# Performance work log

Hardware: AMD Instinct MI355X
Metric: run time of the kernel (lower is better)

Reference implementation:

```python
import jax, jax.numpy as jnp
import numpy as np

MASK_RADIUS = 30.0

def _fft_mask(height, width, mode):
    # replicates fft_filter_def: grid over full H rows and rfft half-plane cols
    cht, cwt = height // 2, width // 2
    fy, fx = jnp.meshgrid(jnp.arange(height), jnp.arange(width // 2 + 1), indexing='ij')
    dist = jnp.sqrt((fx - cwt).astype(jnp.float32) ** 2 + (fy - cht).astype(jnp.float32) ** 2)
    if mode == 'high':
        return (dist > MASK_RADIUS).astype(jnp.float32)
    return (dist <= MASK_RADIUS).astype(jnp.float32)


def setup_inputs() -> dict:
    key = jax.random.key(0)
    k1, k2, k3 = jax.random.split(key, 3)
    B, Cin, Cout, H, W, K = 4, 64, 64, 128, 128, 3
    x = jax.random.normal(k1, (B, Cin, H, W), dtype=jnp.float32)
    weight = jax.random.normal(k2, (Cout, Cin, K, K), dtype=jnp.float32) * 0.1
    bias = jax.random.normal(k3, (Cout,), dtype=jnp.float32) * 0.1
    return {"x": x, "weight": weight, "bias": bias}


def reference(x, weight, bias):
    B, Cin, H, W = x.shape
    x = x.astype(jnp.float32)
    # rfft2 of input, then fftshift (as in original; kernel FFT is NOT shifted)
    fft_x = jnp.fft.rfft2(x)                          # [B, Cin, H, W//2+1]
    fft_x = jnp.fft.fftshift(fft_x, axes=(-2, -1))
    kernel_fft = jnp.fft.rfft2(weight, s=(H, W))      # [Cout, Cin, H, W//2+1]
    # high-pass frequency mask (fft_filter == 'high')
    mask = _fft_mask(H, W, 'high')                    # [H, W//2+1]
    fft_x = fft_x * mask
    # per-frequency complex GEMV over in_channels (avoids [B,Cout,Cin,H,Wf] blowup)
    fft_out = jnp.einsum('bihw,oihw->bohw', fft_x, kernel_fft)
    out = jnp.fft.irfft2(fft_out, s=(H, W))           # [B, Cout, H, W]
    return out + bias[None, :, None, None]
```

## Files before the change

### kernel.cpp

```cpp
#include <hip/hip_runtime.h>

#define PI_F 3.14159265358979323846f

#define HH 128
#define WW 128
#define WF 65
#define NB 4
#define NC 64
#define CPLX_PER_IMG (HH * WF)

typedef __attribute__((ext_vector_type(8))) short short8;
typedef __attribute__((ext_vector_type(4))) float f32x4;

__device__ __forceinline__ ushort f2b(float f) {
    unsigned u = __float_as_uint(f);
    u += 0x7fffu + ((u >> 16) & 1u);
    return (ushort)(u >> 16);
}


__global__ __launch_bounds__(256) void k_pre(const float* __restrict__ w,
                                             ushort* __restrict__ A1,
                                             ushort* __restrict__ A2,
                                             ushort* __restrict__ A4,
                                             ushort* __restrict__ A5,
                                             ushort* __restrict__ WvRe,
                                             ushort* __restrict__ WvIm) {
    int idx = blockIdx.x * 256 + threadIdx.x;
    if (idx < 20480) {
        int m = idx >> 7, k = idx & 127;
        int part = m / 80, v = m - part * 80;
        float s, c;
        __sincosf(2.f * PI_F * (float)((v * k) & 127) / 128.f, &s, &c);
        float val = (v < 65) ? (part ? -s : c) : 0.f;
        A1[idx] = f2b(val);
    } else if (idx < 86016) {
        int j = idx - 20480;
        int m = j >> 8, k2 = j & 255;
        int part = m >> 7, u = m & 127;
        int kp = k2 >> 7, h = k2 & 127;
        float s, c;
        __sincosf(2.f * PI_F * (float)((u * h) & 127) / 128.f, &s, &c);
        float val = part == 0 ? (kp == 0 ? c : s) : (kp == 0 ? -s : c);
        A2[j] = f2b(val);
    } else if (idx < 151552) {
        int j = idx - 86016;
        int m = j >> 8, k2 = j & 255;
        int part = m >> 7, h = m & 127;
        int kp = k2 >> 7, u = k2 & 127;
        float s, c;
        __sincosf(2.f * PI_F * (float)((u * h) & 127) / 128.f, &s, &c);
        float val = part == 0 ? (kp == 0 ? c : -s) : (kp == 0 ? s : c);
        A4[j] = f2b(val * (1.f / 128.f));
    } else if (idx < 172032) {
        int j = idx - 151552;
        int x = j / 160, k2 = j - x * 160;
        int part = k2 / 80, v = k2 - part * 80;
        float s, c;
        __sincosf(2.f * PI_F * (float)((v * x) & 127) / 128.f, &s, &c);
        float cv = (v == 0 || v == 64) ? 1.f : 2.f;
        float val = (v < 65) ? (part == 0 ? cv * c : -cv * s) * (1.f / 128.f) : 0.f;
        A5[j] = f2b(val);
    } else {
        int xw = idx - 172032;
        int i = xw & 63;
        int o = (xw >> 6) & 63;
        int pv = xw >> 12;
        int p = pv / WF;
        int v = pv % WF;
        const float* wp = w + ((size_t)o * 64 + i) * 9 + p * 3;
        float re = wp[0], im = 0.f;
#pragma unroll
        for (int q = 1; q <= 2; ++q) {
            int k = (v * q) & 127;
            float s, c;
            __sincosf(-2.f * PI_F * (float)k / 128.f, &s, &c);
            re += wp[q] * c;
            im += wp[q] * s;
        }
        WvRe[xw] = f2b(re);
        WvIm[xw] = f2b(im);
    }
}

#define B1P 136
#define B2P 280
__global__ __launch_bounds__(1024) void k_fwd(const float* __restrict__ x,
                                              const ushort* __restrict__ A1,
                                              const ushort* __restrict__ A2,
                                              ushort* __restrict__ XsRe,
                                              ushort* __restrict__ XsIm) {
    __shared__ ushort B1[128 * B1P];
    __shared__ ushort B2[80 * B2P];
    int t = threadIdx.x;
    int img = blockIdx.x;
    const float* gx = x + (size_t)img * 16384;
    for (int c = t; c < 2048; c += 1024) {
        int r = c >> 4, sl = c & 15;
        const float* src = gx + r * 128 + sl * 8;
        float4 f0 = *(const float4*)src;
        float4 f1 = *(const float4*)(src + 4);
        short8 v8;
        v8[0] = (short)f2b(f0.x); v8[1] = (short)f2b(f0.y);
        v8[2] = (short)f2b(f0.z); v8[3] = (short)f2b(f0.w);
        v8[4] = (short)f2b(f1.x); v8[5] = (short)f2b(f1.y);
        v8[6] = (short)f2b(f1.z); v8[7] = (short)f2b(f1.w);
        *(short8*)&B1[r * B1P + sl * 8] = v8;
    }
    __syncthreads();
    int lane = t & 63, wave = t >> 6;
    int lrow = lane & 15, lq = lane >> 4;

    {
        int g = wave >> 3, nt = wave & 7;
        int hrow = nt * 16 + lrow;
        f32x4 acc[5];
#pragma unroll
        for (int j = 0; j < 5; ++j) acc[j] = (f32x4){0.f, 0.f, 0.f, 0.f};
#pragma unroll
        for (int ks = 0; ks < 4; ++ks) {
            short8 b = *(short8*)&B1[hrow * B1P + ks * 32 + lq * 8];
#pragma unroll
            for (int j = 0; j < 5; ++j) {
                int mt = g * 5 + j;
                short8 a = *(const short8*)&A1[(mt * 16 + lrow) * 128 + ks * 32 + lq * 8];
                acc[j] = __builtin_amdgcn_mfma_f32_16x16x32_bf16(a, b, acc[j], 0, 0, 0);
            }
        }
#pragma unroll
        for (int j = 0; j < 5; ++j) {
            int m0 = (g * 5 + j) * 16 + lq * 4;
            int part = m0 >= 80;
            int v0 = m0 - part * 80;
#pragma unroll
            for (int e = 0; e < 4; ++e)
                B2[(v0 + e) * B2P + part * 128 + hrow] = f2b(acc[j][e]);
        }
    }
    __syncthreads();

    {
        int nt = wave;
        f32x4 acc[5];
#pragma unroll
        for (int mt = 0; mt < 5; ++mt) acc[mt] = (f32x4){0.f, 0.f, 0.f, 0.f};
#pragma unroll
        for (int ks = 0; ks < 8; ++ks) {
            short8 b = *(const short8*)&A2[(nt * 16 + lrow) * 256 + ks * 32 + lq * 8];
#pragma unroll
            for (int mt = 0; mt < 5; ++mt) {
                short8 a = *(short8*)&B2[(mt * 16 + lrow) * B2P + ks * 32 + lq * 8];
                acc[mt] = __builtin_amdgcn_mfma_f32_16x16x32_bf16(a, b, acc[mt], 0, 0, 0);
            }
        }
        int part = nt >= 8;
        int u = (nt & 7) * 16 + lrow;
        int u_out = (u + 64) & 127;
        int du = u_out - 64;
        ushort* dimg = (part ? XsIm : XsRe) + (size_t)img * CPLX_PER_IMG;
#pragma unroll
        for (int mt = 0; mt < 5; ++mt)
#pragma unroll
            for (int e = 0; e < 4; ++e) {
                int v_in = mt * 16 + lq * 4 + e;
                if (v_in < 65) {
                    int v_out = v_in + 32; if (v_out >= 65) v_out -= 65;
                    int dv = v_out - 64;
                    bool keep = (du * du + dv * dv) > 900;
                    dimg[v_out * 128 + u_out] = keep ? f2b(acc[mt][e]) : (ushort)0;
                }
            }
    }
}

#define AP 72
__global__ __launch_bounds__(256, 2) void k_gemm(const ushort* __restrict__ XsRe,
                                                 const ushort* __restrict__ XsIm,
                                                 const ushort* __restrict__ WvRe,
                                                 const ushort* __restrict__ WvIm,
                                                 ushort* __restrict__ Zre,
                                                 ushort* __restrict__ Zim) {
    __shared__ ushort XTre[128 * AP], XTim[128 * AP];
    __shared__ ushort WSre[64 * AP],  WSim[64 * AP];
    int t = threadIdx.x;
    int v = blockIdx.x >> 2;
    int b = blockIdx.x & 3;
    {
        int u = t & 127, qh = t >> 7;
#pragma unroll
        for (int q8 = 0; q8 < 8; ++q8) {
            int q = qh * 8 + q8;
            ushort re4[4], im4[4];
#pragma unroll
            for (int c = 0; c < 4; ++c) {
                int i = q * 4 + c;
                size_t off = ((size_t)(b * 64 + i) * WF + v) * 128 + u;
                re4[c] = XsRe[off];
                im4[c] = XsIm[off];
            }
            *(ushort4*)&XTre[u * AP + q * 4] = make_ushort4(re4[0], re4[1], re4[2], re4[3]);
            *(ushort4*)&XTim[u * AP + q * 4] = make_ushort4(im4[0], im4[1], im4[2], im4[3]);
        }
    }
    int lane = t & 63, wave = t >> 6;
    int lrow = lane & 15, lq = lane >> 4;
    int u0 = wave * 32;
    f32x4 fRe[8], fIm[8];
#pragma unroll
    for (int m = 0; m < 8; ++m) {
        fRe[m] = (f32x4){0.f, 0.f, 0.f, 0.f};
        fIm[m] = (f32x4){0.f, 0.f, 0.f, 0.f};
    }
    for (int p = 0; p < 3; ++p) {
        if (p) __syncthreads();
        {
            const ushort* gr = WvRe + ((size_t)(p * WF + v)) * 4096;
            const ushort* gi = WvIm + ((size_t)(p * WF + v)) * 4096;
#pragma unroll
            for (int cc = 0; cc < 2; ++cc) {
                int c = t + cc * 256;
                int o = c >> 3, i0 = (c & 7) * 8;
                *(short8*)&WSre[o * AP + i0] = *(const short8*)&gr[c * 8];
                *(short8*)&WSim[o * AP + i0] = *(const short8*)&gi[c * 8];
            }
        }
        __syncthreads();
        f32x4 pRe[8], pIm[8];
#pragma unroll
        for (int m = 0; m < 8; ++m) {
            pRe[m] = (f32x4){0.f, 0.f, 0.f, 0.f};
            pIm[m] = (f32x4){0.f, 0.f, 0.f, 0.f};
        }
#pragma unroll
        for (int ks = 0; ks < 2; ++ks) {
            int kb = ks * 32 + lq * 8;
            short8 br[2], bi[2], bin[2];
#pragma unroll
            for (int ut = 0; ut < 2; ++ut) {
                int u = u0 + ut * 16 + lrow;
                br[ut] = *(const short8*)&XTre[u * AP + kb];
                bi[ut] = *(const short8*)&XTim[u * AP + kb];
                bin[ut] = bi[ut] ^ (short)0x8000;
            }
#pragma unroll
            for (int ot = 0; ot < 4; ++ot) {
                int o = ot * 16 + lrow;
                short8 ar = *(const short8*)&WSre[o * AP + kb];
                short8 ai = *(const short8*)&WSim[o * AP + kb];
#pragma unroll
                for (int ut = 0; ut < 2; ++ut) {
                    int m = ot * 2 + ut;
                    pRe[m] = __builtin_amdgcn_mfma_f32_16x16x32_bf16(ai, bin[ut], pRe[m], 0, 0, 0);
                    pRe[m] = __builtin_amdgcn_mfma_f32_16x16x32_bf16(ar, br[ut],  pRe[m], 0, 0, 0);
                    pIm[m] = __builtin_amdgcn_mfma_f32_16x16x32_bf16(ai, br[ut],  pIm[m], 0, 0, 0);
                    pIm[m] = __builtin_amdgcn_mfma_f32_16x16x32_bf16(ar, bi[ut],  pIm[m], 0, 0, 0);
                }
            }
        }
#pragma unroll
        for (int ut = 0; ut < 2; ++ut) {
            int u = u0 + ut * 16 + lrow;
            float sn, cn;
            __sincosf(-2.f * PI_F * (float)(u * p) / 128.f, &sn, &cn);
#pragma unroll
            for (int ot = 0; ot < 4; ++ot) {
                int m = ot * 2 + ut;
#pragma unroll
                for (int e = 0; e < 4; ++e) {
                    fRe[m][e] += pRe[m][e] * cn - pIm[m][e] * sn;
                    fIm[m][e] += pIm[m][e] * cn + pRe[m][e] * sn;
                }
            }
        }
    }
#pragma unroll
    for (int ot = 0; ot < 4; ++ot)
#pragma unroll
        for (int ut = 0; ut < 2; ++ut) {
            int m = ot * 2 + ut;
            int u = u0 + ut * 16 + lrow;
#pragma unroll
            for (int e = 0; e < 4; ++e) {
                int o = ot * 16 + lq * 4 + e;
                size_t idx = ((size_t)(b * 64 + o) * 65 + v) * 128 + u;
                Zre[idx] = f2b(fRe[m][e]);
                Zim[idx] = f2b(fIm[m][e]);
            }
        }
}

#define B3P 168
__global__ __launch_bounds__(1024) void k_inv(const ushort* __restrict__ Zre,
                                              const ushort* __restrict__ Zim,
                                              const ushort* __restrict__ A4,
                                              const ushort* __restrict__ A5,
                                              const float* __restrict__ bias,
                                              float* __restrict__ out) {
    __shared__ ushort B1[80 * B2P];
    __shared__ ushort B2[128 * B3P];
    int t = threadIdx.x;
    int ch = blockIdx.x;
    for (int c = t; c < 2080; c += 1024) {
        int r = c >> 5, sl = c & 31;
        const ushort* src = (sl < 16 ? Zre : Zim) + ((size_t)ch * 65 + r) * 128 + (sl & 15) * 8;
        *(short8*)&B1[r * B2P + sl * 8] = *(const short8*)src;
    }
    if (t < 480) {
        int r = 65 + (t >> 5), sl = t & 31;
        short8 z = {0, 0, 0, 0, 0, 0, 0, 0};
        *(short8*)&B1[r * B2P + sl * 8] = z;
    }
    __syncthreads();
    int lane = t & 63, wave = t >> 6;
    int lrow = lane & 15, lq = lane >> 4;

    {
        int mt = wave;
        f32x4 acc[5];
#pragma unroll
        for (int nt = 0; nt < 5; ++nt) acc[nt] = (f32x4){0.f, 0.f, 0.f, 0.f};
#pragma unroll
        for (int ks = 0; ks < 8; ++ks) {
            short8 a = *(const short8*)&A4[(mt * 16 + lrow) * 256 + ks * 32 + lq * 8];
#pragma unroll
            for (int nt = 0; nt < 5; ++nt) {
                short8 b = *(short8*)&B1[(nt * 16 + lrow) * B2P + ks * 32 + lq * 8];
                acc[nt] = __builtin_amdgcn_mfma_f32_16x16x32_bf16(a, b, acc[nt], 0, 0, 0);
            }
        }
        int part = mt >= 8;
        int h0 = mt * 16 + lq * 4 - part * 128;
#pragma unroll
        for (int nt = 0; nt < 5; ++nt) {
            int v = nt * 16 + lrow;
#pragma unroll
            for (int e = 0; e < 4; ++e)
                B2[(h0 + e) * B3P + part * 80 + v] = f2b(acc[nt][e]);
        }
    }
    __syncthreads();

    {
        int mt = wave & 7, nh = wave >> 3;
        f32x4 acc[4];
#pragma unroll
        for (int jn = 0; jn < 4; ++jn) acc[jn] = (f32x4){0.f, 0.f, 0.f, 0.f};
#pragma unroll
        for (int ks = 0; ks < 5; ++ks) {
            short8 a = *(short8*)&B2[(mt * 16 + lrow) * B3P + ks * 32 + lq * 8];
#pragma unroll
            for (int jn = 0; jn < 4; ++jn) {
                int nt = nh * 4 + jn;
                short8 b = *(const short8*)&A5[(nt * 16 + lrow) * 160 + ks * 32 + lq * 8];
                acc[jn] = __builtin_amdgcn_mfma_f32_16x16x32_bf16(a, b, acc[jn], 0, 0, 0);
            }
        }
        float bo = bias[ch & 63];
        float* go = out + (size_t)ch * 16384;
#pragma unroll
        for (int jn = 0; jn < 4; ++jn) {
            int xx = (nh * 4 + jn) * 16 + lrow;
#pragma unroll
            for (int e = 0; e < 4; ++e) {
                int h = mt * 16 + lq * 4 + e;
                go[h * 128 + xx] = acc[jn][e] + bo;
            }
        }
    }
}

extern "C" void kernel_launch(void* const* d_in, const int* in_sizes, int n_in,
                              void* d_out, int out_size, void* d_ws, size_t ws_size,
                              hipStream_t stream) {
    const float* x = (const float*)d_in[0];
    const float* w = (const float*)d_in[1];
    const float* bias = (const float*)d_in[2];
    float* out = (float*)d_out;

    char* ws = (char*)d_ws;
    ushort* A1   = (ushort*)(ws + 0);
    ushort* A2   = (ushort*)(ws + 40960);
    ushort* A4   = (ushort*)(ws + 172032);
    ushort* A5   = (ushort*)(ws + 303104);
    ushort* WvRe = (ushort*)(ws + 344064);
    ushort* WvIm = (ushort*)(ws + 1941504);
    ushort* XsRe = (ushort*)(ws + 12058624);
    ushort* XsIm = (ushort*)(ws + 16318464);
    ushort* Zre  = (ushort*)(ws + 20578304);
    ushort* Zim  = (ushort*)(ws + 24838144);

    k_pre<<<3792, 256, 0, stream>>>(w, A1, A2, A4, A5, WvRe, WvIm);
    k_fwd<<<NB * NC, 1024, 0, stream>>>(x, A1, A2, XsRe, XsIm);
    k_gemm<<<WF * NB, 256, 0, stream>>>(XsRe, XsIm, WvRe, WvIm, Zre, Zim);
    k_inv<<<NB * NC, 1024, 0, stream>>>(Zre, Zim, A4, A5, bias, out);
}
```

Baseline: 54.21 us.

## Fuse precompute kernel into forward FFT kernel, generate twiddles on the fly

```diff
diff --git a/kernel.cpp b/kernel.cpp
--- a/kernel.cpp
+++ b/kernel.cpp
@@ -19,31 +19,12 @@
 }
 
 
-__global__ __launch_bounds__(256) void k_pre(const float* __restrict__ w,
-                                             ushort* __restrict__ A1,
-                                             ushort* __restrict__ A2,
-                                             ushort* __restrict__ A4,
-                                             ushort* __restrict__ A5,
-                                             ushort* __restrict__ WvRe,
-                                             ushort* __restrict__ WvIm) {
-    int idx = blockIdx.x * 256 + threadIdx.x;
-    if (idx < 20480) {
-        int m = idx >> 7, k = idx & 127;
-        int part = m / 80, v = m - part * 80;
-        float s, c;
-        __sincosf(2.f * PI_F * (float)((v * k) & 127) / 128.f, &s, &c);
-        float val = (v < 65) ? (part ? -s : c) : 0.f;
-        A1[idx] = f2b(val);
-    } else if (idx < 86016) {
-        int j = idx - 20480;
-        int m = j >> 8, k2 = j & 255;
-        int part = m >> 7, u = m & 127;
-        int kp = k2 >> 7, h = k2 & 127;
-        float s, c;
-        __sincosf(2.f * PI_F * (float)((u * h) & 127) / 128.f, &s, &c);
-        float val = part == 0 ? (kp == 0 ? c : s) : (kp == 0 ? -s : c);
-        A2[j] = f2b(val);
-    } else if (idx < 151552) {
+__device__ __forceinline__ void pre_item_tail(int idx, const float* __restrict__ w,
+                                              ushort* __restrict__ A4,
+                                              ushort* __restrict__ A5,
+                                              ushort* __restrict__ WvRe,
+                                              ushort* __restrict__ WvIm) {
+    if (idx < 151552) {
         int j = idx - 86016;
         int m = j >> 8, k2 = j & 255;
         int part = m >> 7, h = m & 127;
@@ -85,16 +66,22 @@
 
 #define B1P 136
 #define B2P 280
+#define A1P 136
 __global__ __launch_bounds__(1024) void k_fwd(const float* __restrict__ x,
-                                              const ushort* __restrict__ A1,
-                                              const ushort* __restrict__ A2,
+                                              const float* __restrict__ w,
                                               ushort* __restrict__ XsRe,
-                                              ushort* __restrict__ XsIm) {
+                                              ushort* __restrict__ XsIm,
+                                              ushort* __restrict__ WvRe,
+                                              ushort* __restrict__ WvIm,
+                                              ushort* __restrict__ A4,
+                                              ushort* __restrict__ A5) {
     __shared__ ushort B1[128 * B1P];
     __shared__ ushort B2[80 * B2P];
+    __shared__ ushort A1L[160 * A1P];
     int t = threadIdx.x;
     int img = blockIdx.x;
     const float* gx = x + (size_t)img * 16384;
+
     for (int c = t; c < 2048; c += 1024) {
         int r = c >> 4, sl = c & 15;
         const float* src = gx + r * 128 + sl * 8;
@@ -107,7 +94,21 @@
         v8[6] = (short)f2b(f1.z); v8[7] = (short)f2b(f1.w);
         *(short8*)&B1[r * B1P + sl * 8] = v8;
     }
+    for (int idx = t; idx < 20480; idx += 1024) {
+        int m = idx >> 7, k = idx & 127;
+        int part = m / 80, v = m - part * 80;
+        float s, c;
+        __sincosf(2.f * PI_F * (float)((v * k) & 127) / 128.f, &s, &c);
+        float val = (v < 65) ? (part ? -s : c) : 0.f;
+        A1L[m * A1P + k] = f2b(val);
+    }
+    {
+        int gtid = img * 1024 + t;
+        for (int idx = 86016 + gtid; idx < 970752; idx += 262144)
+            pre_item_tail(idx, w, A4, A5, WvRe, WvIm);
+    }
     __syncthreads();
+
     int lane = t & 63, wave = t >> 6;
     int lrow = lane & 15, lq = lane >> 4;
 
@@ -123,7 +124,7 @@
 #pragma unroll
             for (int j = 0; j < 5; ++j) {
                 int mt = g * 5 + j;
-                short8 a = *(const short8*)&A1[(mt * 16 + lrow) * 128 + ks * 32 + lq * 8];
+                short8 a = *(const short8*)&A1L[(mt * 16 + lrow) * A1P + ks * 32 + lq * 8];
                 acc[j] = __builtin_amdgcn_mfma_f32_16x16x32_bf16(a, b, acc[j], 0, 0, 0);
             }
         }
@@ -141,19 +142,30 @@
 
     {
         int nt = wave;
+        int part = nt >= 8;
+        int um = (nt & 7) * 16 + lrow;
         f32x4 acc[5];
 #pragma unroll
         for (int mt = 0; mt < 5; ++mt) acc[mt] = (f32x4){0.f, 0.f, 0.f, 0.f};
 #pragma unroll
         for (int ks = 0; ks < 8; ++ks) {
-            short8 b = *(const short8*)&A2[(nt * 16 + lrow) * 256 + ks * 32 + lq * 8];
+            int kp = ks >> 2;
+            int hbase = (ks & 3) * 32 + lq * 8;
+            short8 bfr;
+#pragma unroll
+            for (int e = 0; e < 8; ++e) {
+                int hh = hbase + e;
+                float s, c;
+                __sincosf(2.f * PI_F * (float)((um * hh) & 127) / 128.f, &s, &c);
+                float val = !part ? (kp == 0 ? c : s) : (kp == 0 ? -s : c);
+                bfr[e] = (short)f2b(val);
+            }
 #pragma unroll
             for (int mt = 0; mt < 5; ++mt) {
                 short8 a = *(short8*)&B2[(mt * 16 + lrow) * B2P + ks * 32 + lq * 8];
-                acc[mt] = __builtin_amdgcn_mfma_f32_16x16x32_bf16(a, b, acc[mt], 0, 0, 0);
-            }
-        }
-        int part = nt >= 8;
+                acc[mt] = __builtin_amdgcn_mfma_f32_16x16x32_bf16(a, bfr, acc[mt], 0, 0, 0);
+            }
+        }
         int u = (nt & 7) * 16 + lrow;
         int u_out = (u + 64) & 127;
         int du = u_out - 64;
@@ -282,7 +294,7 @@
 #pragma unroll
             for (int e = 0; e < 4; ++e) {
                 int o = ot * 16 + lq * 4 + e;
-                size_t idx = ((size_t)(b * 64 + o) * 65 + v) * 128 + u;
+                size_t idx = ((size_t)(b * 64 + o) * WF + v) * 128 + u;
                 Zre[idx] = f2b(fRe[m][e]);
                 Zim[idx] = f2b(fIm[m][e]);
             }
@@ -302,7 +314,7 @@
     int ch = blockIdx.x;
     for (int c = t; c < 2080; c += 1024) {
         int r = c >> 5, sl = c & 31;
-        const ushort* src = (sl < 16 ? Zre : Zim) + ((size_t)ch * 65 + r) * 128 + (sl & 15) * 8;
+        const ushort* src = (sl < 16 ? Zre : Zim) + ((size_t)ch * WF + r) * 128 + (sl & 15) * 8;
         *(short8*)&B1[r * B2P + sl * 8] = *(const short8*)src;
     }
     if (t < 480) {
@@ -378,8 +390,6 @@
     float* out = (float*)d_out;
 
     char* ws = (char*)d_ws;
-    ushort* A1   = (ushort*)(ws + 0);
-    ushort* A2   = (ushort*)(ws + 40960);
     ushort* A4   = (ushort*)(ws + 172032);
     ushort* A5   = (ushort*)(ws + 303104);
     ushort* WvRe = (ushort*)(ws + 344064);
@@ -389,8 +399,7 @@
     ushort* Zre  = (ushort*)(ws + 20578304);
     ushort* Zim  = (ushort*)(ws + 24838144);
 
-    k_pre<<<3792, 256, 0, stream>>>(w, A1, A2, A4, A5, WvRe, WvIm);
-    k_fwd<<<NB * NC, 1024, 0, stream>>>(x, A1, A2, XsRe, XsIm);
+    k_fwd<<<NB * NC, 1024, 0, stream>>>(x, w, XsRe, XsIm, WvRe, WvIm, A4, A5);
     k_gemm<<<WF * NB, 256, 0, stream>>>(XsRe, XsIm, WvRe, WvIm, Zre, Zim);
     k_inv<<<NB * NC, 1024, 0, stream>>>(Zre, Zim, A4, A5, bias, out);
 }
```

Result: faster. 47.13 us (-13.1%).
